# Kernel optimization log

Measured on AMD Instinct MI355X. Metric: run time of the kernel, lower is better.

The kernel has to match this reference:

```python
import jax, jax.numpy as jnp
import numpy as np

N_NODES = 50000
N_EDGES = 800000
K_HOPS = 4
F_IN, F_HID, A_DIM = 6, 128, 3


def gcn_norm(edge_index, edge_weight, num_nodes):
    # TAGConv(normalize=True) uses gcn_norm WITHOUT added self-loops:
    # norm = D^{-1/2}[src] * w * D^{-1/2}[dst], deg computed at target (col).
    row, col = edge_index[0], edge_index[1]
    deg = jax.ops.segment_sum(edge_weight, col, num_segments=num_nodes)
    deg_inv_sqrt = jnp.where(deg > 0, jax.lax.rsqrt(deg), 0.0)
    return deg_inv_sqrt[row] * edge_weight * deg_inv_sqrt[col]


def tag_conv(x, edge_index, norm_w, W, b):
    # out = sum_{k=0..K} (A_hat^k x) @ W[k] + b ; W: [K+1, in, out]
    row, col = edge_index[0], edge_index[1]
    out = x @ W[0]
    xk = x
    for k in range(1, W.shape[0]):
        # one sparse propagation hop: gather at src, scale, scatter-add at dst
        xk = jax.ops.segment_sum(norm_w[:, None] * xk[row], col, num_segments=x.shape[0])
        out = out + xk @ W[k]
    return out + b


def setup_inputs() -> dict:
    key = jax.random.key(0)
    ks = jax.random.split(key, 5)
    x = jax.random.normal(ks[0], (N_NODES, F_IN), dtype=jnp.float32)
    edge_index = jax.random.randint(ks[1], (2, N_EDGES), 0, N_NODES, dtype=jnp.int32)
    edge_weight = jax.random.uniform(ks[2], (N_EDGES,), dtype=jnp.float32)
    s1 = float(1.0 / np.sqrt(F_IN))
    s2 = float(1.0 / np.sqrt(F_HID))
    W1 = jax.random.uniform(ks[3], (K_HOPS + 1, F_IN, F_HID), minval=-s1, maxval=s1, dtype=jnp.float32)
    b1 = jnp.zeros((F_HID,), jnp.float32)
    W2 = jax.random.uniform(ks[4], (K_HOPS + 1, F_HID, 2 * A_DIM), minval=-s2, maxval=s2, dtype=jnp.float32)
    b2 = jnp.zeros((2 * A_DIM,), jnp.float32)
    return {"x": x, "edge_index": edge_index, "edge_weight": edge_weight,
            "W1": W1, "b1": b1, "W2": W2, "b2": b2}


def reference(x, edge_index, edge_weight, W1, b1, W2, b2):
    norm_w = gcn_norm(edge_index, edge_weight, x.shape[0])
    h = jax.nn.relu(tag_conv(x, edge_index, norm_w, W1, b1))
    out = tag_conv(h, edge_index, norm_w, W2, b2)
    mu = jnp.tanh(out[..., :A_DIM])
    logvar = jnp.tanh(out[..., A_DIM:])
    sigma = jnp.exp(2.0 * logvar)
    return mu, sigma
```

## Files before the change

### kernel.cpp

```cpp
#include <hip/hip_runtime.h>

#define NN 50000
#define NE 800000
#define KH 4
#define FIN 6
#define FH 128
#define FO 6
#define ADIM 3
#define NN6 (NN * 6)
#define NBKT 196
#define EPB 2048
#define NPB 391
#define CAP 5120
#define ROWMASK 0xFFFFFu
#define GFUSE 2048

typedef unsigned int u32;

struct __align__(8) Edge { u32 r; float w; };

__global__ void bucket_hist(const int* __restrict__ col, u32* __restrict__ ghist) {
    __shared__ u32 h[NBKT];
    for (int t = threadIdx.x; t < NBKT; t += 256) h[t] = 0;
    __syncthreads();
    int base = blockIdx.x * EPB;
#pragma unroll
    for (int i = 0; i < EPB / 256; ++i) {
        int e = base + i * 256 + threadIdx.x;
        if (e < NE) atomicAdd(&h[((u32)col[e]) >> 8], 1u);
    }
    __syncthreads();
    for (int t = threadIdx.x; t < NBKT; t += 256)
        if (h[t]) atomicAdd(&ghist[t], h[t]);
}

__global__ void bucket_scan(const u32* __restrict__ ghist, u32* __restrict__ bbase,
                            u32* __restrict__ bcur, int* __restrict__ offs) {
    __shared__ u32 sh[256];
    int t = threadIdx.x;
    u32 v = (t < NBKT) ? ghist[t] : 0;
    sh[t] = v;
    __syncthreads();
    for (int off = 1; off < 256; off <<= 1) {
        u32 u = (t >= off) ? sh[t - off] : 0;
        __syncthreads();
        sh[t] += u;
        __syncthreads();
    }
    if (t < NBKT) { bbase[t] = sh[t] - v; bcur[t] = sh[t] - v; }
    if (t == NBKT - 1) bbase[NBKT] = sh[t];
    if (t == 0) offs[NN] = NE;
}

__global__ __launch_bounds__(256) void partition_kernel(
        const int* __restrict__ row, const int* __restrict__ col,
        const float* __restrict__ w, u32* __restrict__ bcur,
        Edge* __restrict__ etmp) {
    __shared__ u32 hcnt[NBKT];
    __shared__ u32 hloc[NBKT];
    __shared__ u32 hglb[NBKT];
    __shared__ u32 smeta[EPB];
    __shared__ float swt[EPB];
    __shared__ u32 sgid[EPB];
    __shared__ u32 sc[256];
    for (int t = threadIdx.x; t < NBKT; t += 256) hcnt[t] = 0;
    __syncthreads();
    int base = blockIdx.x * EPB;
    u32 m_[8]; float w_[8]; u32 b_[8]; u32 rk_[8]; int v_[8];
#pragma unroll
    for (int i = 0; i < 8; ++i) {
        int e = base + i * 256 + threadIdx.x;
        v_[i] = e < NE;
        if (v_[i]) {
            u32 c = (u32)col[e];
            u32 r = (u32)row[e];
            b_[i] = c >> 8;
            m_[i] = ((c & 255u) << 20) | r;
            w_[i] = w[e];
            rk_[i] = atomicAdd(&hcnt[b_[i]], 1u);
        }
    }
    __syncthreads();
    {
        int t = threadIdx.x;
        u32 v = (t < NBKT) ? hcnt[t] : 0;
        sc[t] = v;
        __syncthreads();
        for (int off = 1; off < 256; off <<= 1) {
            u32 u = (t >= off) ? sc[t - off] : 0;
            __syncthreads();
            sc[t] += u;
            __syncthreads();
        }
        if (t < NBKT) hloc[t] = sc[t] - v;
    }
    __syncthreads();
    for (int t = threadIdx.x; t < NBKT; t += 256)
        if (hcnt[t]) hglb[t] = atomicAdd(&bcur[t], hcnt[t]);
    __syncthreads();
#pragma unroll
    for (int i = 0; i < 8; ++i) if (v_[i]) {
        u32 slot = hloc[b_[i]] + rk_[i];
        smeta[slot] = m_[i];
        swt[slot] = w_[i];
        sgid[slot] = hglb[b_[i]] + rk_[i];
    }
    __syncthreads();
    int tot = NE - base; if (tot > EPB) tot = EPB;
    for (int s = threadIdx.x; s < tot; s += 256) {
        Edge ed; ed.r = smeta[s]; ed.w = swt[s];
        etmp[sgid[s]] = ed;
    }
}

__global__ __launch_bounds__(256) void bucket_csr(
        const u32* __restrict__ bbase, const Edge* __restrict__ etmp,
        Edge* __restrict__ edges, int* __restrict__ offs,
        float* __restrict__ dinv) {
    int b = blockIdx.x;
    int t = threadIdx.x;
    u32 s = bbase[b], e = bbase[b + 1];
    int cnt = (int)(e - s);
    int node0 = b << 8;
    int nloc = NN - node0; if (nloc > 256) nloc = 256;
    __shared__ u32 ncnt[256];
    __shared__ float nsum[256];
    __shared__ u32 ncur[256];
    __shared__ u32 sc[256];
    __shared__ Edge stage[CAP];
    ncnt[t] = 0; nsum[t] = 0.f;
    __syncthreads();
    for (int i = t; i < cnt; i += 256) {
        Edge ed = etmp[s + i];
        u32 cl = ed.r >> 20;
        atomicAdd(&ncnt[cl], 1u);
        atomicAdd(&nsum[cl], ed.w);
    }
    __syncthreads();
    u32 v = ncnt[t];
    sc[t] = v;
    __syncthreads();
    for (int off = 1; off < 256; off <<= 1) {
        u32 u = (t >= off) ? sc[t - off] : 0;
        __syncthreads();
        sc[t] += u;
        __syncthreads();
    }
    u32 excl = sc[t] - v;
    ncur[t] = excl;
    if (t < nloc) {
        offs[node0 + t] = (int)(s + excl);
        float d = nsum[t];
        dinv[node0 + t] = d > 0.f ? rsqrtf(d) : 0.f;
    }
    __syncthreads();
    for (int i = t; i < cnt; i += 256) {
        Edge ed = etmp[s + i];
        u32 cl = ed.r >> 20;
        u32 slot = atomicAdd(&ncur[cl], 1u);
        Edge ce; ce.r = ed.r & ROWMASK; ce.w = ed.w;
        if (slot < CAP) stage[slot] = ce;
        else edges[s + slot] = ce;
    }
    __syncthreads();
    int lim = cnt < CAP ? cnt : CAP;
    for (int i = t; i < lim; i += 256) edges[s + i] = stage[i];
}

__global__ void hop8_norm(const int* __restrict__ offs, Edge* __restrict__ edges,
                          const float* __restrict__ dinv, const float* __restrict__ xprev,
                          float* __restrict__ xnext) {
    int t = blockIdx.x * blockDim.x + threadIdx.x;
    int n = t >> 3, j = t & 7;
    if (n >= NN) return;
    int s = offs[n], e = offs[n + 1];
    float dn = dinv[n];
    float a0 = 0.f, a1 = 0.f, a2 = 0.f, a3 = 0.f, a4 = 0.f, a5 = 0.f;
    for (int i = s + j; i < e; i += 8) {
        Edge ed = edges[i];
        float wn = ed.w * dn * dinv[ed.r];
        ed.w = wn;
        edges[i] = ed;
        const float* xr = xprev + (size_t)ed.r * 6;
        a0 += wn * xr[0]; a1 += wn * xr[1]; a2 += wn * xr[2];
        a3 += wn * xr[3]; a4 += wn * xr[4]; a5 += wn * xr[5];
    }
#pragma unroll
    for (int d = 1; d < 8; d <<= 1) {
        a0 += __shfl_xor(a0, d); a1 += __shfl_xor(a1, d); a2 += __shfl_xor(a2, d);
        a3 += __shfl_xor(a3, d); a4 += __shfl_xor(a4, d); a5 += __shfl_xor(a5, d);
    }
    if (j < 6) {
        float v = j == 0 ? a0 : j == 1 ? a1 : j == 2 ? a2 : j == 3 ? a3 : j == 4 ? a4 : a5;
        xnext[n * 6 + j] = v;
    }
}

__global__ void hop8(const int* __restrict__ offs, const Edge* __restrict__ edges,
                     const float* __restrict__ xprev, int xst, int xof,
                     const float* __restrict__ yadd,
                     float* __restrict__ xnext) {
    int t = blockIdx.x * blockDim.x + threadIdx.x;
    int n = t >> 3, j = t & 7;
    if (n >= NN) return;
    int s = offs[n], e = offs[n + 1];
    float a0 = 0.f, a1 = 0.f, a2 = 0.f, a3 = 0.f, a4 = 0.f, a5 = 0.f;
    for (int i = s + j; i < e; i += 8) {
        Edge ed = edges[i];
        const float* xr = xprev + (size_t)ed.r * xst + xof;
        a0 += ed.w * xr[0]; a1 += ed.w * xr[1]; a2 += ed.w * xr[2];
        a3 += ed.w * xr[3]; a4 += ed.w * xr[4]; a5 += ed.w * xr[5];
    }
#pragma unroll
    for (int d = 1; d < 8; d <<= 1) {
        a0 += __shfl_xor(a0, d); a1 += __shfl_xor(a1, d); a2 += __shfl_xor(a2, d);
        a3 += __shfl_xor(a3, d); a4 += __shfl_xor(a4, d); a5 += __shfl_xor(a5, d);
    }
    if (j < 6) {
        float v = j == 0 ? a0 : j == 1 ? a1 : j == 2 ? a2 : j == 3 ? a3 : j == 4 ? a4 : a5;
        if (yadd) v += yadd[(size_t)n * 30 + j];
        xnext[n * 6 + j] = v;
    }
}

__global__ void hop8_final(const int* __restrict__ offs, const Edge* __restrict__ edges,
                           const float* __restrict__ xprev, const float* __restrict__ y0,
                           float* __restrict__ out) {
    int t = blockIdx.x * blockDim.x + threadIdx.x;
    int n = t >> 3, j = t & 7;
    if (n >= NN) return;
    int s = offs[n], e = offs[n + 1];
    float a0 = 0.f, a1 = 0.f, a2 = 0.f, a3 = 0.f, a4 = 0.f, a5 = 0.f;
    for (int i = s + j; i < e; i += 8) {
        Edge ed = edges[i];
        const float* xr = xprev + (size_t)ed.r * 6;
        a0 += ed.w * xr[0]; a1 += ed.w * xr[1]; a2 += ed.w * xr[2];
        a3 += ed.w * xr[3]; a4 += ed.w * xr[4]; a5 += ed.w * xr[5];
    }
#pragma unroll
    for (int d = 1; d < 8; d <<= 1) {
        a0 += __shfl_xor(a0, d); a1 += __shfl_xor(a1, d); a2 += __shfl_xor(a2, d);
        a3 += __shfl_xor(a3, d); a4 += __shfl_xor(a4, d); a5 += __shfl_xor(a5, d);
    }
    if (j < 6) {
        float v = j == 0 ? a0 : j == 1 ? a1 : j == 2 ? a2 : j == 3 ? a3 : j == 4 ? a4 : a5;
        v += y0[(size_t)n * 30 + j];
        float tv = tanhf(v);
        if (j < ADIM) out[n * ADIM + j] = tv;
        else          out[NN * ADIM + n * ADIM + (j - ADIM)] = expf(2.f * tv);
    }
}

__global__ __launch_bounds__(256) void fused_dense_kernel(
        const float* __restrict__ x, const float* __restrict__ xs,
        const float* __restrict__ W1, const float* __restrict__ b1,
        const float* __restrict__ W2, const float* __restrict__ b2,
        float* __restrict__ ys) {
    __shared__ float sin_[2][32];
    __shared__ float sh[2][128];
    int t = threadIdx.x;
    int f = t & 127, half = t >> 7;
    float w1r[30];
#pragma unroll
    for (int i = 0; i < 30; ++i) w1r[i] = W1[i * FH + f];
    float b1r = b1[f];
    bool bact = t < 240;
    int bn = t / 120;
    int rem = t % 120;
    int ka = rem >> 2;
    int q  = rem & 3;
    int k2 = ka / 6, a2 = ka - k2 * 6;
    float w2r[32];
#pragma unroll
    for (int i = 0; i < 32; ++i)
        w2r[i] = bact ? W2[((size_t)k2 * FH + q * 32 + i) * FO + a2] : 0.f;
    float badd = (bact && k2 == 0 && q == 0) ? b2[a2] : 0.f;

    for (int n0 = blockIdx.x * 2; n0 < NN; n0 += GFUSE * 2) {
        if (t < 60) {
            int nn = t / 30, c = t - nn * 30;
            int n = n0 + nn;
            float v;
            if (c < 6) v = x[n * 6 + c];
            else       v = xs[(size_t)((c - 6) / 6) * NN6 + n * 6 + (c - 6) % 6];
            sin_[nn][c] = v;
        }
        __syncthreads();
        {
            float s = b1r;
#pragma unroll
            for (int i = 0; i < 30; ++i) s += sin_[half][i] * w1r[i];
            sh[half][f] = s > 0.f ? s : 0.f;
        }
        __syncthreads();
        if (bact) {
            float s = badd;
            const float* hr = &sh[bn][q * 32];
#pragma unroll
            for (int i = 0; i < 32; ++i) s += hr[i] * w2r[i];
            s += __shfl_xor(s, 1);
            s += __shfl_xor(s, 2);
            if (q == 0) ys[(size_t)(n0 + bn) * 30 + ka] = s;
        }
    }
}

extern "C" void kernel_launch(void* const* d_in, const int* in_sizes, int n_in,
                              void* d_out, int out_size, void* d_ws, size_t ws_size,
                              hipStream_t stream) {
    const float* x  = (const float*)d_in[0];
    const int*   ei = (const int*)d_in[1];
    const float* ew = (const float*)d_in[2];
    const float* W1 = (const float*)d_in[3];
    const float* b1 = (const float*)d_in[4];
    const float* W2 = (const float*)d_in[5];
    const float* b2 = (const float*)d_in[6];
    float* out = (float*)d_out;

    const int* row = ei;
    const int* col = ei + NE;

    Edge*  etmp  = (Edge*)d_ws;
    Edge*  edges = etmp + NE;
    u32*   ghist = (u32*)(edges + NE);
    u32*   bbase = ghist + NBKT;
    u32*   bcur  = bbase + NBKT + 1;
    int*   offs  = (int*)(bcur + NBKT);
    float* dinv  = (float*)(offs + NN + 1);
    float* xs    = dinv + NN;
    float* ys    = xs + (size_t)KH * NN6;
    float* za    = ys + (size_t)NN * 30;
    float* zb    = za + NN6;

    const int B = 256;
    const int gHop = (NN * 8 + B - 1) / B;

    hipMemsetAsync(ghist, 0, NBKT * sizeof(u32), stream);
    bucket_hist<<<NPB, B, 0, stream>>>(col, ghist);
    bucket_scan<<<1, B, 0, stream>>>(ghist, bbase, bcur, offs);
    partition_kernel<<<NPB, B, 0, stream>>>(row, col, ew, bcur, etmp);
    bucket_csr<<<NBKT, B, 0, stream>>>(bbase, etmp, edges, offs, dinv);

    hop8_norm<<<gHop, B, 0, stream>>>(offs, edges, dinv, x, xs);
    for (int k = 2; k <= KH; ++k)
        hop8<<<gHop, B, 0, stream>>>(offs, edges,
                                     xs + (size_t)(k - 2) * NN6, 6, 0, nullptr,
                                     xs + (size_t)(k - 1) * NN6);

    fused_dense_kernel<<<GFUSE, B, 0, stream>>>(x, xs, W1, b1, W2, b2, ys);

    hop8<<<gHop, B, 0, stream>>>(offs, edges, ys, 30, 24, ys + 18, za);
    hop8<<<gHop, B, 0, stream>>>(offs, edges, za, 6, 0, ys + 12, zb);
    hop8<<<gHop, B, 0, stream>>>(offs, edges, zb, 6, 0, ys + 6, za);
    hop8_final<<<gHop, B, 0, stream>>>(offs, edges, za, ys, out);
}
```

Measured before the change: 164.5 us.

## Pad node features to 8 floats and pad CSR rows to even length for vector loads

Node feature buffers switch from a stride of 6 to 8 floats (and ys from 30 to 32), so each gather becomes a float4 plus a float2 load. CSR rows are padded to an even edge count with zero-weight dummy edges, so each lane can read two edges as one int4, and a separate end-offset array is added. The intent is to cut the number of memory instructions in the gather-bound hop kernels. In exchange it adds a pad_x kernel, more memory traffic for the padded features and dummy edges, and each hop thread now walks its row in strides of 16.

Result: no change. 166.5 us (+1.2%).

```diff
diff --git a/kernel.cpp b/kernel.cpp
--- a/kernel.cpp
+++ b/kernel.cpp
@@ -8,12 +8,14 @@
 #define FO 6
 #define ADIM 3
 #define NN6 (NN * 6)
+#define NN8 (NN * 8)
 #define NBKT 196
 #define EPB 2048
 #define NPB 391
 #define CAP 5120
 #define ROWMASK 0xFFFFFu
 #define GFUSE 2048
+#define NEPAD (NE + NBKT * 256)
 
 typedef unsigned int u32;
 
@@ -35,7 +37,7 @@
 }
 
 __global__ void bucket_scan(const u32* __restrict__ ghist, u32* __restrict__ bbase,
-                            u32* __restrict__ bcur, int* __restrict__ offs) {
+                            u32* __restrict__ bcur) {
     __shared__ u32 sh[256];
     int t = threadIdx.x;
     u32 v = (t < NBKT) ? ghist[t] : 0;
@@ -49,7 +51,6 @@
     }
     if (t < NBKT) { bbase[t] = sh[t] - v; bcur[t] = sh[t] - v; }
     if (t == NBKT - 1) bbase[NBKT] = sh[t];
-    if (t == 0) offs[NN] = NE;
 }
 
 __global__ __launch_bounds__(256) void partition_kernel(
@@ -115,12 +116,13 @@
 
 __global__ __launch_bounds__(256) void bucket_csr(
         const u32* __restrict__ bbase, const Edge* __restrict__ etmp,
-        Edge* __restrict__ edges, int* __restrict__ offs,
+        Edge* __restrict__ edges, int* __restrict__ offs, int* __restrict__ eoff,
         float* __restrict__ dinv) {
     int b = blockIdx.x;
     int t = threadIdx.x;
     u32 s = bbase[b], e = bbase[b + 1];
     int cnt = (int)(e - s);
+    u32 rb = s + (u32)b * 256u;
     int node0 = b << 8;
     int nloc = NN - node0; if (nloc > 256) nloc = 256;
     __shared__ u32 ncnt[256];
@@ -138,7 +140,8 @@
     }
     __syncthreads();
     u32 v = ncnt[t];
-    sc[t] = v;
+    u32 pv = (v + 1u) & ~1u;
+    sc[t] = pv;
     __syncthreads();
     for (int off = 1; off < 256; off <<= 1) {
         u32 u = (t >= off) ? sc[t - off] : 0;
@@ -146,10 +149,12 @@
         sc[t] += u;
         __syncthreads();
     }
-    u32 excl = sc[t] - v;
+    u32 excl = sc[t] - pv;
+    u32 ptot = sc[255];
     ncur[t] = excl;
     if (t < nloc) {
-        offs[node0 + t] = (int)(s + excl);
+        offs[node0 + t] = (int)(rb + excl);
+        eoff[node0 + t] = (int)(rb + excl + pv);
         float d = nsum[t];
         dinv[node0 + t] = d > 0.f ? rsqrtf(d) : 0.f;
     }
@@ -160,56 +165,51 @@
         u32 slot = atomicAdd(&ncur[cl], 1u);
         Edge ce; ce.r = ed.r & ROWMASK; ce.w = ed.w;
         if (slot < CAP) stage[slot] = ce;
-        else edges[s + slot] = ce;
-    }
-    __syncthreads();
-    int lim = cnt < CAP ? cnt : CAP;
-    for (int i = t; i < lim; i += 256) edges[s + i] = stage[i];
-}
-
-__global__ void hop8_norm(const int* __restrict__ offs, Edge* __restrict__ edges,
-                          const float* __restrict__ dinv, const float* __restrict__ xprev,
-                          float* __restrict__ xnext) {
+        else edges[rb + slot] = ce;
+    }
+    if (t < nloc && (v & 1u)) {
+        u32 slot = excl + v;
+        Edge ce; ce.r = 0u; ce.w = 0.f;
+        if (slot < CAP) stage[slot] = ce;
+        else edges[rb + slot] = ce;
+    }
+    __syncthreads();
+    int lim = (int)(ptot < CAP ? ptot : CAP);
+    for (int i = t; i < lim; i += 256) edges[rb + i] = stage[i];
+}
+
+__global__ void pad_x(const float* __restrict__ x, float* __restrict__ xpad) {
     int t = blockIdx.x * blockDim.x + threadIdx.x;
-    int n = t >> 3, j = t & 7;
-    if (n >= NN) return;
-    int s = offs[n], e = offs[n + 1];
-    float dn = dinv[n];
-    float a0 = 0.f, a1 = 0.f, a2 = 0.f, a3 = 0.f, a4 = 0.f, a5 = 0.f;
-    for (int i = s + j; i < e; i += 8) {
-        Edge ed = edges[i];
-        float wn = ed.w * dn * dinv[ed.r];
-        ed.w = wn;
-        edges[i] = ed;
-        const float* xr = xprev + (size_t)ed.r * 6;
-        a0 += wn * xr[0]; a1 += wn * xr[1]; a2 += wn * xr[2];
-        a3 += wn * xr[3]; a4 += wn * xr[4]; a5 += wn * xr[5];
-    }
-#pragma unroll
-    for (int d = 1; d < 8; d <<= 1) {
-        a0 += __shfl_xor(a0, d); a1 += __shfl_xor(a1, d); a2 += __shfl_xor(a2, d);
-        a3 += __shfl_xor(a3, d); a4 += __shfl_xor(a4, d); a5 += __shfl_xor(a5, d);
-    }
-    if (j < 6) {
-        float v = j == 0 ? a0 : j == 1 ? a1 : j == 2 ? a2 : j == 3 ? a3 : j == 4 ? a4 : a5;
-        xnext[n * 6 + j] = v;
-    }
-}
-
-__global__ void hop8(const int* __restrict__ offs, const Edge* __restrict__ edges,
+    if (t >= NN8) return;
+    int n = t >> 3, c = t & 7;
+    xpad[t] = (c < 6) ? x[n * 6 + c] : 0.f;
+}
+
+__device__ __forceinline__ void gather6(const float* __restrict__ base, u32 r,
+                                        int xst, int xof, float w,
+                                        float& a0, float& a1, float& a2,
+                                        float& a3, float& a4, float& a5) {
+    const float* xr = base + (size_t)r * xst + xof;
+    float4 u = *(const float4*)xr;
+    float2 v = *(const float2*)(xr + 4);
+    a0 += w * u.x; a1 += w * u.y; a2 += w * u.z;
+    a3 += w * u.w; a4 += w * v.x; a5 += w * v.y;
+}
+
+__global__ void hop8(const int* __restrict__ offs, const int* __restrict__ eoff,
+                     const Edge* __restrict__ edges,
                      const float* __restrict__ xprev, int xst, int xof,
                      const float* __restrict__ yadd,
                      float* __restrict__ xnext) {
     int t = blockIdx.x * blockDim.x + threadIdx.x;
     int n = t >> 3, j = t & 7;
     if (n >= NN) return;
-    int s = offs[n], e = offs[n + 1];
+    int s = offs[n], e = eoff[n];
     float a0 = 0.f, a1 = 0.f, a2 = 0.f, a3 = 0.f, a4 = 0.f, a5 = 0.f;
-    for (int i = s + j; i < e; i += 8) {
-        Edge ed = edges[i];
-        const float* xr = xprev + (size_t)ed.r * xst + xof;
-        a0 += ed.w * xr[0]; a1 += ed.w * xr[1]; a2 += ed.w * xr[2];
-        a3 += ed.w * xr[3]; a4 += ed.w * xr[4]; a5 += ed.w * xr[5];
+    for (int i = s + 2 * j; i < e; i += 16) {
+        int4 ep = *(const int4*)&edges[i];
+        gather6(xprev, (u32)ep.x, xst, xof, __int_as_float(ep.y), a0, a1, a2, a3, a4, a5);
+        gather6(xprev, (u32)ep.z, xst, xof, __int_as_float(ep.w), a0, a1, a2, a3, a4, a5);
     }
 #pragma unroll
     for (int d = 1; d < 8; d <<= 1) {
@@ -218,24 +218,55 @@
     }
     if (j < 6) {
         float v = j == 0 ? a0 : j == 1 ? a1 : j == 2 ? a2 : j == 3 ? a3 : j == 4 ? a4 : a5;
-        if (yadd) v += yadd[(size_t)n * 30 + j];
-        xnext[n * 6 + j] = v;
-    }
-}
-
-__global__ void hop8_final(const int* __restrict__ offs, const Edge* __restrict__ edges,
+        if (yadd) v += yadd[(size_t)n * 32 + j];
+        xnext[n * 8 + j] = v;
+    }
+}
+
+__global__ void hop8_norm(const int* __restrict__ offs, const int* __restrict__ eoff,
+                          Edge* __restrict__ edges,
+                          const float* __restrict__ dinv, const float* __restrict__ xpad,
+                          float* __restrict__ xnext) {
+    int t = blockIdx.x * blockDim.x + threadIdx.x;
+    int n = t >> 3, j = t & 7;
+    if (n >= NN) return;
+    int s = offs[n], e = eoff[n];
+    float dn = dinv[n];
+    float a0 = 0.f, a1 = 0.f, a2 = 0.f, a3 = 0.f, a4 = 0.f, a5 = 0.f;
+    for (int i = s + 2 * j; i < e; i += 16) {
+        int4 ep = *(const int4*)&edges[i];
+        u32 r0 = (u32)ep.x, r1 = (u32)ep.z;
+        float wn0 = __int_as_float(ep.y) * dn * dinv[r0];
+        float wn1 = __int_as_float(ep.w) * dn * dinv[r1];
+        ep.y = __float_as_int(wn0); ep.w = __float_as_int(wn1);
+        *(int4*)&edges[i] = ep;
+        gather6(xpad, r0, 8, 0, wn0, a0, a1, a2, a3, a4, a5);
+        gather6(xpad, r1, 8, 0, wn1, a0, a1, a2, a3, a4, a5);
+    }
+#pragma unroll
+    for (int d = 1; d < 8; d <<= 1) {
+        a0 += __shfl_xor(a0, d); a1 += __shfl_xor(a1, d); a2 += __shfl_xor(a2, d);
+        a3 += __shfl_xor(a3, d); a4 += __shfl_xor(a4, d); a5 += __shfl_xor(a5, d);
+    }
+    if (j < 6) {
+        float v = j == 0 ? a0 : j == 1 ? a1 : j == 2 ? a2 : j == 3 ? a3 : j == 4 ? a4 : a5;
+        xnext[n * 8 + j] = v;
+    }
+}
+
+__global__ void hop8_final(const int* __restrict__ offs, const int* __restrict__ eoff,
+                           const Edge* __restrict__ edges,
                            const float* __restrict__ xprev, const float* __restrict__ y0,
                            float* __restrict__ out) {
     int t = blockIdx.x * blockDim.x + threadIdx.x;
     int n = t >> 3, j = t & 7;
     if (n >= NN) return;
-    int s = offs[n], e = offs[n + 1];
+    int s = offs[n], e = eoff[n];
     float a0 = 0.f, a1 = 0.f, a2 = 0.f, a3 = 0.f, a4 = 0.f, a5 = 0.f;
-    for (int i = s + j; i < e; i += 8) {
-        Edge ed = edges[i];
-        const float* xr = xprev + (size_t)ed.r * 6;
-        a0 += ed.w * xr[0]; a1 += ed.w * xr[1]; a2 += ed.w * xr[2];
-        a3 += ed.w * xr[3]; a4 += ed.w * xr[4]; a5 += ed.w * xr[5];
+    for (int i = s + 2 * j; i < e; i += 16) {
+        int4 ep = *(const int4*)&edges[i];
+        gather6(xprev, (u32)ep.x, 8, 0, __int_as_float(ep.y), a0, a1, a2, a3, a4, a5);
+        gather6(xprev, (u32)ep.z, 8, 0, __int_as_float(ep.w), a0, a1, a2, a3, a4, a5);
     }
 #pragma unroll
     for (int d = 1; d < 8; d <<= 1) {
@@ -244,7 +275,7 @@
     }
     if (j < 6) {
         float v = j == 0 ? a0 : j == 1 ? a1 : j == 2 ? a2 : j == 3 ? a3 : j == 4 ? a4 : a5;
-        v += y0[(size_t)n * 30 + j];
+        v += y0[(size_t)n * 32 + j];
         float tv = tanhf(v);
         if (j < ADIM) out[n * ADIM + j] = tv;
         else          out[NN * ADIM + n * ADIM + (j - ADIM)] = expf(2.f * tv);
@@ -282,7 +313,7 @@
             int n = n0 + nn;
             float v;
             if (c < 6) v = x[n * 6 + c];
-            else       v = xs[(size_t)((c - 6) / 6) * NN6 + n * 6 + (c - 6) % 6];
+            else       v = xs[(size_t)((c - 6) / 6) * NN8 + n * 8 + (c - 6) % 6];
             sin_[nn][c] = v;
         }
         __syncthreads();
@@ -300,7 +331,7 @@
             for (int i = 0; i < 32; ++i) s += hr[i] * w2r[i];
             s += __shfl_xor(s, 1);
             s += __shfl_xor(s, 2);
-            if (q == 0) ys[(size_t)(n0 + bn) * 30 + ka] = s;
+            if (q == 0) ys[(size_t)(n0 + bn) * 32 + ka] = s;
         }
     }
 }
@@ -322,35 +353,39 @@
 
     Edge*  etmp  = (Edge*)d_ws;
     Edge*  edges = etmp + NE;
-    u32*   ghist = (u32*)(edges + NE);
+    float* xpad  = (float*)(edges + NEPAD);
+    float* xs    = xpad + NN8;
+    float* ys    = xs + (size_t)KH * NN8;
+    float* za    = ys + (size_t)NN * 32;
+    float* zb    = za + NN8;
+    u32*   ghist = (u32*)(zb + NN8);
     u32*   bbase = ghist + NBKT;
     u32*   bcur  = bbase + NBKT + 1;
     int*   offs  = (int*)(bcur + NBKT);
-    float* dinv  = (float*)(offs + NN + 1);
-    float* xs    = dinv + NN;
-    float* ys    = xs + (size_t)KH * NN6;
-    float* za    = ys + (size_t)NN * 30;
-    float* zb    = za + NN6;
+    int*   eoff  = offs + NN;
+    float* dinv  = (float*)(eoff + NN);
 
     const int B = 256;
     const int gHop = (NN * 8 + B - 1) / B;
+    const int gPad = (NN8 + B - 1) / B;
 
     hipMemsetAsync(ghist, 0, NBKT * sizeof(u32), stream);
     bucket_hist<<<NPB, B, 0, stream>>>(col, ghist);
-    bucket_scan<<<1, B, 0, stream>>>(ghist, bbase, bcur, offs);
+    bucket_scan<<<1, B, 0, stream>>>(ghist, bbase, bcur);
     partition_kernel<<<NPB, B, 0, stream>>>(row, col, ew, bcur, etmp);
-    bucket_csr<<<NBKT, B, 0, stream>>>(bbase, etmp, edges, offs, dinv);
-
-    hop8_norm<<<gHop, B, 0, stream>>>(offs, edges, dinv, x, xs);
+    bucket_csr<<<NBKT, B, 0, stream>>>(bbase, etmp, edges, offs, eoff, dinv);
+    pad_x<<<gPad, B, 0, stream>>>(x, xpad);
+
+    hop8_norm<<<gHop, B, 0, stream>>>(offs, eoff, edges, dinv, xpad, xs);
     for (int k = 2; k <= KH; ++k)
-        hop8<<<gHop, B, 0, stream>>>(offs, edges,
-                                     xs + (size_t)(k - 2) * NN6, 6, 0, nullptr,
-                                     xs + (size_t)(k - 1) * NN6);
+        hop8<<<gHop, B, 0, stream>>>(offs, eoff, edges,
+                                     xs + (size_t)(k - 2) * NN8, 8, 0, nullptr,
+                                     xs + (size_t)(k - 1) * NN8);
 
     fused_dense_kernel<<<GFUSE, B, 0, stream>>>(x, xs, W1, b1, W2, b2, ys);
 
-    hop8<<<gHop, B, 0, stream>>>(offs, edges, ys, 30, 24, ys + 18, za);
-    hop8<<<gHop, B, 0, stream>>>(offs, edges, za, 6, 0, ys + 12, zb);
-    hop8<<<gHop, B, 0, stream>>>(offs, edges, zb, 6, 0, ys + 6, za);
-    hop8_final<<<gHop, B, 0, stream>>>(offs, edges, za, ys, out);
-}
+    hop8<<<gHop, B, 0, stream>>>(offs, eoff, edges, ys, 32, 24, ys + 18, za);
+    hop8<<<gHop, B, 0, stream>>>(offs, eoff, edges, za, 8, 0, ys + 12, zb);
+    hop8<<<gHop, B, 0, stream>>>(offs, eoff, edges, zb, 8, 0, ys + 6, za);
+    hop8_final<<<gHop, B, 0, stream>>>(offs, eoff, edges, za, ys, out);
+}
```
